# Performance work log

Measured on AMD Instinct MI355X. Metric: run time of the kernel, lower is better.

## Reference

```python
import jax, jax.numpy as jnp
import numpy as np
import math

N_HEAD = 16
V_HEAD = 32   # v_head_dim
NOPE = 32     # nope_head_dim
ROPE_D = 64   # rope_head_dim
KEEP = 256    # num_tokens_to_keep
EPS = 1e-6


def _freqs(T, dim=ROPE_D, theta=10000.0):
    f = 1.0 / (theta ** (jnp.arange(0, dim, 2, dtype=jnp.float32) / dim))
    t = jnp.arange(T, dtype=jnp.float32)
    a = jnp.outer(t, f)  # [T, dim//2]
    return jnp.cos(a), jnp.sin(a)


def _rope(x, cos, sin):
    # x: [B,H,S,D]; half-split rotation as in apply_rope
    S = x.shape[-2]
    c = cos[:S][None, None]
    s = sin[:S][None, None]
    x1, x2 = jnp.split(x, 2, axis=-1)
    return jnp.concatenate([x1 * c - x2 * s, x1 * s + x2 * c], axis=-1)


def _rms(x, g, eps=EPS):
    return x * jax.lax.rsqrt(jnp.mean(x * x, axis=-1, keepdims=True) + eps) * g


def _attn(q, k, v, causal):
    scale = 1.0 / math.sqrt(q.shape[-1])
    s = jnp.einsum('bhqd,bhkd->bhqk', q, k) * scale
    if causal:
        Tq, Tk = s.shape[-2], s.shape[-1]
        mask = jnp.tril(jnp.ones((Tq, Tk), dtype=bool))
        s = jnp.where(mask, s, jnp.finfo(s.dtype).min)
    return jnp.einsum('bhqk,bhkd->bhqd', jax.nn.softmax(s, axis=-1), v)


def _forward(x, w_cq, g_qnorm, w_dq_nope, w_dq_rope, w_ckv, g_kvnorm,
             w_dk_nope, w_dv, w_krope, w_imp, w_selk, w_selv,
             w_wink, w_winv, w_gate, w_proj):
    B, T, C = x.shape
    cos, sin = _freqs(T)

    # --- MLA query path ---
    nq = _rms(x @ w_cq, g_qnorm)                                  # [B,T,96]
    q_nope = (nq @ w_dq_nope).reshape(B, T, N_HEAD, NOPE).transpose(0, 2, 1, 3)
    q_rope = (nq @ w_dq_rope).reshape(B, T, N_HEAD, ROPE_D).transpose(0, 2, 1, 3)
    q_rope = _rope(q_rope, cos, sin)
    q = jnp.concatenate([q_nope, q_rope], axis=-1)                # [B,H,T,96]

    # --- branch gate ---
    gate = jax.nn.softmax((x @ w_gate).mean(axis=1), axis=-1)     # [B,3]

    # --- branch 1: MLA-compressed full KV ---
    ckv = _rms(x @ w_ckv, g_kvnorm)                               # [B,T,32]
    k_nope = (ckv @ w_dk_nope).reshape(B, T, N_HEAD, NOPE).transpose(0, 2, 1, 3)
    v1 = (ckv @ w_dv).reshape(B, T, N_HEAD, V_HEAD).transpose(0, 2, 1, 3)
    k_rope = (x @ w_krope).reshape(B, T, 1, ROPE_D).transpose(0, 2, 1, 3) / N_HEAD
    k_rope = _rope(k_rope, cos, sin)
    k1 = jnp.concatenate(
        [k_nope, jnp.broadcast_to(k_rope, (B, N_HEAD, T, ROPE_D))], axis=-1)

    # --- branch 2: top-k selected tokens ---
    scores = (x @ w_imp)[..., 0]                                  # [B,T]
    _, idx = jax.lax.top_k(scores, KEEP)
    idx = jnp.sort(idx, axis=1)
    sel = jnp.take_along_axis(x, idx[:, :, None], axis=1)         # [B,S,C]
    ks = (sel @ w_selk).reshape(B, KEEP, N_HEAD, NOPE + ROPE_D).transpose(0, 2, 1, 3)
    vs = (sel @ w_selv).reshape(B, KEEP, N_HEAD, V_HEAD).transpose(0, 2, 1, 3)
    ks = jnp.concatenate([ks[..., :NOPE], _rope(ks[..., NOPE:], cos, sin)], axis=-1)

    # --- branch 3: sliding window (training mode -> full x) ---
    kw = (x @ w_wink).reshape(B, T, N_HEAD, NOPE + ROPE_D).transpose(0, 2, 1, 3)
    vw = (x @ w_winv).reshape(B, T, N_HEAD, V_HEAD).transpose(0, 2, 1, 3)
    kw = jnp.concatenate([kw[..., :NOPE], _rope(kw[..., NOPE:], cos, sin)], axis=-1)

    a1 = _attn(q, k1, v1, causal=True)
    a2 = _attn(q, ks, vs, causal=False)
    a3 = _attn(q, kw, vw, causal=True)

    g = gate[:, :, None, None, None]
    out = g[:, 0] * a1 + g[:, 1] * a2 + g[:, 2] * a3              # [B,H,T,Vd]
    out = out.transpose(0, 2, 1, 3).reshape(B, T, N_HEAD * V_HEAD)
    return out @ w_proj                                           # [B,T,C]


def setup_inputs() -> dict:
    key = jax.random.key(0)
    ks = jax.random.split(key, 20)
    B, T, C = 2, 1024, 1024
    q_lora, kv_lora = 96, 32
    std = 0.02
    def w(k, shape):
        return jax.random.normal(k, shape, dtype=jnp.float32) * std
    return {
        'x': jax.random.normal(ks[0], (B, T, C), dtype=jnp.float32),
        'w_cq': w(ks[1], (C, q_lora)),
        'g_qnorm': jnp.ones((q_lora,), jnp.float32),
        'w_dq_nope': w(ks[2], (q_lora, N_HEAD * NOPE)),
        'w_dq_rope': w(ks[3], (q_lora, N_HEAD * ROPE_D)),
        'w_ckv': w(ks[4], (C, kv_lora)),
        'g_kvnorm': jnp.ones((kv_lora,), jnp.float32),
        'w_dk_nope': w(ks[5], (kv_lora, N_HEAD * NOPE)),
        'w_dv': w(ks[6], (kv_lora, N_HEAD * V_HEAD)),
        'w_krope': w(ks[7], (C, ROPE_D)),
        'w_imp': w(ks[8], (C, 1)),
        'w_selk': w(ks[9], (C, N_HEAD * (NOPE + ROPE_D))),
        'w_selv': w(ks[10], (C, N_HEAD * V_HEAD)),
        'w_wink': w(ks[11], (C, N_HEAD * (NOPE + ROPE_D))),
        'w_winv': w(ks[12], (C, N_HEAD * V_HEAD)),
        'w_gate': w(ks[13], (C, 3)),
        'w_proj': w(ks[14], (N_HEAD * V_HEAD, C)),
    }


def reference(x, w_cq, g_qnorm, w_dq_nope, w_dq_rope, w_ckv, g_kvnorm,
              w_dk_nope, w_dv, w_krope, w_imp, w_selk, w_selv,
              w_wink, w_winv, w_gate, w_proj):
    return _forward(x, w_cq, g_qnorm, w_dq_nope, w_dq_rope, w_ckv, g_kvnorm,
                    w_dk_nope, w_dv, w_krope, w_imp, w_selk, w_selv,
                    w_wink, w_winv, w_gate, w_proj)
```

## Files before the change

kernel.cpp:

```cpp
#include <hip/hip_runtime.h>
#include <math.h>

#define T_SEQ   1024
#define BATCH   2
#define CDIM    1024
#define NHEAD   16
#define VHEAD   32
#define KEEP    256
#define HEAD_D  96
#define SCALE_ATTN 0.1020620726159658f

#define BQ   64
#define BKT  64
#define SK   100
#define SPT  66
#define SPV  36

#define GBK 16
#define SA  132

#define XWW    2244
#define C_CQ   0
#define C_CKV  96
#define C_KRO  128
#define C_WINK 192
#define C_WINV 1728
#define C_IMP  2240
#define C_GATE 2241

#define QKVW   2560
#define C_QN   0
#define C_QR   512
#define C_KN   1536
#define C_V1   2048

#define SKW  2048

__global__ __launch_bounds__(256) void gemm128(const float* __restrict__ A,
                                               const float* __restrict__ B,
                                               float* __restrict__ C,
                                               int M, int N, int K,
                                               int lda, int ldb, int ldc,
                                               int kchunk) {
    __shared__ float As[GBK][SA];
    __shared__ float Bs[GBK][SA];
    int t = threadIdx.x;
    int tx = t & 15, ty = t >> 4;
    int row0 = blockIdx.y * 128, col0 = blockIdx.x * 128;
    int kb = blockIdx.z * kchunk;
    int ke = min(K, kb + kchunk);
    float acc[8][8] = {};

    for (int k0 = kb; k0 < ke; k0 += GBK) {
#pragma unroll
        for (int r = 0; r < 2; r++) {
            int idx = t + 256 * r;
            int row = idx >> 2, k4 = idx & 3;
            int gr = row0 + row;
            float4 v = make_float4(0.f, 0.f, 0.f, 0.f);
            if (gr < M) v = *(const float4*)&A[(size_t)gr * lda + k0 + k4 * 4];
            As[k4 * 4 + 0][row] = v.x;
            As[k4 * 4 + 1][row] = v.y;
            As[k4 * 4 + 2][row] = v.z;
            As[k4 * 4 + 3][row] = v.w;
        }
#pragma unroll
        for (int r = 0; r < 2; r++) {
            int idx = t + 256 * r;
            int kk = idx >> 5, n4 = idx & 31;
            int gc = col0 + n4 * 4;
            float4 v = make_float4(0.f, 0.f, 0.f, 0.f);
            if (gc + 3 < N) {
                v = *(const float4*)&B[(size_t)(k0 + kk) * ldb + gc];
            } else if (gc < N) {
                const float* bp = &B[(size_t)(k0 + kk) * ldb];
                float tmp[4] = {0.f, 0.f, 0.f, 0.f};
                for (int j = 0; j < 4 && gc + j < N; j++) tmp[j] = bp[gc + j];
                v = make_float4(tmp[0], tmp[1], tmp[2], tmp[3]);
            }
            *(float4*)&Bs[kk][n4 * 4] = v;
        }
        __syncthreads();
#pragma unroll
        for (int kk = 0; kk < GBK; kk++) {
            float4 a0 = *(float4*)&As[kk][ty * 4];
            float4 a1 = *(float4*)&As[kk][64 + ty * 4];
            float4 b0 = *(float4*)&Bs[kk][tx * 4];
            float4 b1 = *(float4*)&Bs[kk][64 + tx * 4];
            float av[8] = {a0.x, a0.y, a0.z, a0.w, a1.x, a1.y, a1.z, a1.w};
            float bv[8] = {b0.x, b0.y, b0.z, b0.w, b1.x, b1.y, b1.z, b1.w};
#pragma unroll
            for (int i = 0; i < 8; i++)
#pragma unroll
                for (int j = 0; j < 8; j++) acc[i][j] += av[i] * bv[j];
        }
        __syncthreads();
    }

    bool split = (gridDim.z > 1);
#pragma unroll
    for (int i = 0; i < 8; i++) {
        int gr = row0 + ((i < 4) ? (ty * 4 + i) : (64 + ty * 4 + (i - 4)));
        if (gr >= M) continue;
#pragma unroll
        for (int half = 0; half < 2; half++) {
            int gc = col0 + half * 64 + tx * 4;
            if (gc + 3 >= N) continue;
            float* cp = &C[(size_t)gr * ldc + gc];
            if (split) {
                atomicAdd(cp + 0, acc[i][half * 4 + 0]);
                atomicAdd(cp + 1, acc[i][half * 4 + 1]);
                atomicAdd(cp + 2, acc[i][half * 4 + 2]);
                atomicAdd(cp + 3, acc[i][half * 4 + 3]);
            } else {
                *(float4*)cp = make_float4(acc[i][half * 4 + 0], acc[i][half * 4 + 1],
                                           acc[i][half * 4 + 2], acc[i][half * 4 + 3]);
            }
        }
    }
}

__global__ void build_tab(float2* __restrict__ tab) {
    int idx = blockIdx.x * blockDim.x + threadIdx.x;
    if (idx >= T_SEQ * 32) return;
    int pos = idx >> 5, i = idx & 31;
    float expo = (float)i * (1.0f / 32.0f);
    float f = 1.0f / powf(10000.0f, expo);
    float a = (float)pos * f;
    float s, c;
    sincosf(a, &s, &c);
    tab[idx] = make_float2(c, s);
}

__global__ void pack_all(float* __restrict__ Bxw, float* __restrict__ Bqkv,
                         float* __restrict__ Bsel,
                         const float* __restrict__ cq, const float* __restrict__ ckv,
                         const float* __restrict__ kro, const float* __restrict__ wink,
                         const float* __restrict__ winv, const float* __restrict__ imp,
                         const float* __restrict__ gate,
                         const float* __restrict__ dqn, const float* __restrict__ dqr,
                         const float* __restrict__ dkn, const float* __restrict__ dv,
                         const float* __restrict__ selk, const float* __restrict__ selv) {
    int blk = blockIdx.x;
    if (blk < 1024) {
        int r = blk;
        for (int c = threadIdx.x; c < XWW; c += blockDim.x) {
            float v;
            if      (c < C_CKV)  v = cq  [(size_t)r * 96   + c];
            else if (c < C_KRO)  v = ckv [(size_t)r * 32   + (c - C_CKV)];
            else if (c < C_WINK) v = kro [(size_t)r * 64   + (c - C_KRO)];
            else if (c < C_WINV) v = wink[(size_t)r * 1536 + (c - C_WINK)];
            else if (c < C_IMP)  v = winv[(size_t)r * 512  + (c - C_WINV)];
            else if (c < C_GATE) v = imp [(size_t)r * 1    + (c - C_IMP)];
            else                 v = gate[(size_t)r * 3    + (c - C_GATE)];
            Bxw[(size_t)r * XWW + c] = v;
        }
    } else if (blk < 1152) {
        int r = blk - 1024;
        for (int c = threadIdx.x; c < QKVW; c += blockDim.x) {
            float v = 0.f;
            if (r < 96) {
                if (c < C_QR)      v = dqn[(size_t)r * 512 + c];
                else if (c < C_KN) v = dqr[(size_t)r * 1024 + (c - C_QR)];
            } else {
                if (c >= C_KN && c < C_V1) v = dkn[(size_t)(r - 96) * 512 + (c - C_KN)];
                else if (c >= C_V1)        v = dv [(size_t)(r - 96) * 512 + (c - C_V1)];
            }
            Bqkv[(size_t)r * QKVW + c] = v;
        }
    } else {
        int r = blk - 1152;
        for (int c = threadIdx.x; c < SKW; c += blockDim.x) {
            float v = (c < 1536) ? selk[(size_t)r * 1536 + c]
                                 : selv[(size_t)r * 512 + (c - 1536)];
            Bsel[(size_t)r * SKW + c] = v;
        }
    }
}

__global__ void xw_post(float* __restrict__ XW, const float* __restrict__ gq,
                        const float* __restrict__ gkv,
                        const float2* __restrict__ tab) {
    int row = blockIdx.x;
    int t = threadIdx.x;
    int w = t >> 6, lane = t & 63;
    float* rp = XW + (size_t)row * XWW;
    int pos = row & (T_SEQ - 1);
    const float2* tp = tab + pos * 32;

    if (w == 0) {
        float ss = 0.f;
        for (int d = lane; d < 96; d += 64) { float v = rp[d]; ss += v * v; }
        for (int off = 32; off; off >>= 1) ss += __shfl_xor(ss, off, 64);
        float r = rsqrtf(ss / 96.0f + 1e-6f);
        for (int d = lane; d < 96; d += 64) rp[d] *= r * gq[d];
    } else if (w == 1) {
        float ss = 0.f;
        for (int d = lane; d < 32; d += 64) { float v = rp[C_CKV + d]; ss += v * v; }
        for (int off = 32; off; off >>= 1) ss += __shfl_xor(ss, off, 64);
        float r = rsqrtf(ss / 32.0f + 1e-6f);
        for (int d = lane; d < 32; d += 64) rp[C_CKV + d] *= r * gkv[d];
    } else if (w == 2) {
        if (lane < 32) {
            float2 cs = tp[lane];
            float v1 = rp[C_KRO + lane], v2 = rp[C_KRO + 32 + lane];
            rp[C_KRO + lane]      = (v1 * cs.x - v2 * cs.y) * (1.0f / NHEAD);
            rp[C_KRO + 32 + lane] = (v1 * cs.y + v2 * cs.x) * (1.0f / NHEAD);
        }
    }
#pragma unroll
    for (int j = 0; j < 2; j++) {
        int item = t + j * 256;
        int h = item >> 5, i = item & 31;
        float2 cs = tp[i];
        size_t base = (size_t)(C_WINK + 32) + h * 96;
        float v1 = rp[base + i], v2 = rp[base + 32 + i];
        rp[base + i]      = v1 * cs.x - v2 * cs.y;
        rp[base + 32 + i] = v1 * cs.y + v2 * cs.x;
    }
}

__global__ void rope_tab(float* __restrict__ buf, int nrows, int rstride,
                         int nheads, int hstride, int roff, int posmod,
                         const float2* __restrict__ tab) {
    int total = nrows * nheads * 32;
    for (int it = blockIdx.x * blockDim.x + threadIdx.x; it < total;
         it += gridDim.x * blockDim.x) {
        int i = it & 31;
        int hr = it >> 5;
        int h = hr % nheads;
        int row = hr / nheads;
        int pos = row % posmod;
        float2 cs = tab[pos * 32 + i];
        size_t base = (size_t)row * rstride + (size_t)h * hstride + roff;
        float v1 = buf[base + i], v2 = buf[base + 32 + i];
        buf[base + i]      = v1 * cs.x - v2 * cs.y;
        buf[base + 32 + i] = v1 * cs.y + v2 * cs.x;
    }
}

__global__ void topk_gate(const float* __restrict__ xw, int* __restrict__ idx,
                          float* __restrict__ gate) {
    int b = blockIdx.x;
    __shared__ float s[1024];
    __shared__ int ps[1024];
    __shared__ float gred[3][16];
    int t = threadIdx.x;
    const float* rowp = &xw[((size_t)b * T_SEQ + t) * XWW];
    s[t] = rowp[C_IMP];
    float g0 = rowp[C_GATE + 0], g1 = rowp[C_GATE + 1], g2 = rowp[C_GATE + 2];
    for (int off = 32; off; off >>= 1) {
        g0 += __shfl_xor(g0, off, 64);
        g1 += __shfl_xor(g1, off, 64);
        g2 += __shfl_xor(g2, off, 64);
    }
    if ((t & 63) == 0) { int w = t >> 6; gred[0][w] = g0; gred[1][w] = g1; gred[2][w] = g2; }
    __syncthreads();
    if (t == 0) {
        float v0 = 0.f, v1 = 0.f, v2 = 0.f;
        for (int w = 0; w < 16; w++) { v0 += gred[0][w]; v1 += gred[1][w]; v2 += gred[2][w]; }
        v0 /= (float)T_SEQ; v1 /= (float)T_SEQ; v2 /= (float)T_SEQ;
        float m = fmaxf(v0, fmaxf(v1, v2));
        float e0 = expf(v0 - m), e1 = expf(v1 - m), e2 = expf(v2 - m);
        float ssum = e0 + e1 + e2;
        gate[b * 3 + 0] = e0 / ssum;
        gate[b * 3 + 1] = e1 / ssum;
        gate[b * 3 + 2] = e2 / ssum;
    }
    __syncthreads();
    float mine = s[t];
    int rank = 0;
    for (int j = 0; j < 1024; j++) {
        float v = s[j];
        rank += (v > mine) || (v == mine && j < t);
    }
    int selv = (rank < KEEP) ? 1 : 0;
    ps[t] = selv;
    __syncthreads();
    for (int off = 1; off < 1024; off <<= 1) {
        int add = (t >= off) ? ps[t - off] : 0;
        __syncthreads();
        ps[t] += add;
        __syncthreads();
    }
    if (selv) idx[b * KEEP + ps[t] - 1] = t;
}

__global__ void gather_sel(const float* __restrict__ x, const int* __restrict__ idx,
                           float* __restrict__ sel) {
    for (size_t i = (size_t)blockIdx.x * blockDim.x + threadIdx.x;
         i < (size_t)BATCH * KEEP * CDIM; i += (size_t)gridDim.x * blockDim.x) {
        int c = (int)(i & (CDIM - 1));
        int r = (int)((i >> 10) & (KEEP - 1));
        int b = (int)(i >> 18);
        sel[i] = x[((size_t)b * T_SEQ + idx[b * KEEP + r]) * CDIM + c];
    }
}

__global__ __launch_bounds__(512, 4) void flash_fused(
    const float* __restrict__ qkv, const float* __restrict__ xw,
    const float* __restrict__ skv, const float* __restrict__ gate,
    float* __restrict__ out) {
    __shared__ float Qs[BQ * SK];
    __shared__ float Ks[BKT * SK];
    __shared__ float Vs[BKT * SPV];
    __shared__ float Pt[BKT * SPT];

    int b = blockIdx.z, h = blockIdx.y;
    int qt = blockIdx.x;
    if (b == 1) qt = (gridDim.x - 1) - qt;
    int q0 = qt * BQ;
    int t = threadIdx.x;
    int tq = t >> 4, tk = t & 15;

    for (int i = t; i < BQ * 24; i += 512) {
        int row = i / 24, d4 = i % 24;
        size_t rq = (size_t)b * T_SEQ + q0 + row;
        float4 v;
        if (d4 < 8) v = *(const float4*)&qkv[rq * QKVW + C_QN + h * 32 + d4 * 4];
        else        v = *(const float4*)&qkv[rq * QKVW + C_QR + h * 64 + (d4 - 8) * 4];
        *(float4*)&Qs[row * SK + d4 * 4] = v;
    }

    int qq0 = q0 + 2 * tq, qq1 = qq0 + 1;
    float comb[2][2] = {};
    for (int phase = 0; phase < 3; phase++) {
        bool causal = (phase != 1);
        int ntiles = causal ? (qt + 1) : (KEEP / BKT);
        float m0 = -1e30f, m1 = -1e30f, l0 = 0.f, l1 = 0.f;
        float o00 = 0.f, o01 = 0.f, o10 = 0.f, o11 = 0.f;

        for (int kt = 0; kt < ntiles; kt++) {
            int j0 = kt * BKT;
            __syncthreads();

            for (int i = t; i < BKT * 24; i += 512) {
                int row = i / 24, d4 = i % 24;
                int j = j0 + row;
                float4 v;
                if (phase == 0) {
                    size_t rk = (size_t)b * T_SEQ + j;
                    if (d4 < 8) v = *(const float4*)&qkv[rk * QKVW + C_KN + h * 32 + d4 * 4];
                    else        v = *(const float4*)&xw[rk * XWW + C_KRO + (d4 - 8) * 4];
                } else if (phase == 1) {
                    v = *(const float4*)&skv[((size_t)b * KEEP + j) * SKW + h * 96 + d4 * 4];
                } else {
                    v = *(const float4*)&xw[((size_t)b * T_SEQ + j) * XWW + C_WINK + h * 96 + d4 * 4];
                }
                *(float4*)&Ks[row * SK + d4 * 4] = v;
            }
            for (int i = t; i < BKT * 8; i += 512) {
                int row = i >> 3, d4 = i & 7;
                int j = j0 + row;
                float4 v;
                if (phase == 0)      v = *(const float4*)&qkv[((size_t)b * T_SEQ + j) * QKVW + C_V1 + h * 32 + d4 * 4];
                else if (phase == 1) v = *(const float4*)&skv[((size_t)b * KEEP  + j) * SKW + 1536 + h * 32 + d4 * 4];
                else                 v = *(const float4*)&xw[((size_t)b * T_SEQ + j) * XWW + C_WINV + h * 32 + d4 * 4];
                *(float4*)&Vs[row * SPV + d4 * 4] = v;
            }
            __syncthreads();

            float s0[4] = {}, s1[4] = {};
#pragma unroll 6
            for (int d = 0; d < HEAD_D; d += 4) {
                float4 qa = *(float4*)&Qs[(2 * tq)     * SK + d];
                float4 qb = *(float4*)&Qs[(2 * tq + 1) * SK + d];
#pragma unroll
                for (int j = 0; j < 4; j++) {
                    float4 kv = *(float4*)&Ks[(16 * j + tk) * SK + d];
                    s0[j] += qa.x * kv.x + qa.y * kv.y + qa.z * kv.z + qa.w * kv.w;
                    s1[j] += qb.x * kv.x + qb.y * kv.y + qb.z * kv.z + qb.w * kv.w;
                }
            }
            float mt0 = -1e30f, mt1 = -1e30f;
#pragma unroll
            for (int j = 0; j < 4; j++) {
                int kk = j0 + 16 * j + tk;
                s0[j] *= SCALE_ATTN;
                s1[j] *= SCALE_ATTN;
                if (causal && kk > qq0) s0[j] = -1e30f;
                if (causal && kk > qq1) s1[j] = -1e30f;
                mt0 = fmaxf(mt0, s0[j]);
                mt1 = fmaxf(mt1, s1[j]);
            }
#pragma unroll
            for (int off = 1; off <= 8; off <<= 1) {
                mt0 = fmaxf(mt0, __shfl_xor(mt0, off, 64));
                mt1 = fmaxf(mt1, __shfl_xor(mt1, off, 64));
            }
            float mn0 = fmaxf(m0, mt0), mn1 = fmaxf(m1, mt1);
            float a0 = __expf(m0 - mn0), a1 = __expf(m1 - mn1);
            m0 = mn0; m1 = mn1;

            float rs0 = 0.f, rs1 = 0.f;
#pragma unroll
            for (int j = 0; j < 4; j++) {
                float p0 = __expf(s0[j] - mn0);
                float p1 = __expf(s1[j] - mn1);
                rs0 += p0; rs1 += p1;
                *(float2*)&Pt[(16 * j + tk) * SPT + 2 * tq] = make_float2(p0, p1);
            }
#pragma unroll
            for (int off = 1; off <= 8; off <<= 1) {
                rs0 += __shfl_xor(rs0, off, 64);
                rs1 += __shfl_xor(rs1, off, 64);
            }
            l0 = l0 * a0 + rs0;
            l1 = l1 * a1 + rs1;

            o00 *= a0; o01 *= a0; o10 *= a1; o11 *= a1;
#pragma unroll 8
            for (int kk = 0; kk < BKT; kk++) {
                float2 pv = *(float2*)&Pt[kk * SPT + 2 * tq];
                float2 vv = *(float2*)&Vs[kk * SPV + 2 * tk];
                o00 += pv.x * vv.x; o01 += pv.x * vv.y;
                o10 += pv.y * vv.x; o11 += pv.y * vv.y;
            }
        }

        float g = gate[b * 3 + phase];
        float i0 = g / l0, i1 = g / l1;
        comb[0][0] += o00 * i0; comb[0][1] += o01 * i0;
        comb[1][0] += o10 * i1; comb[1][1] += o11 * i1;
    }

    size_t r0 = ((size_t)b * T_SEQ + q0 + 2 * tq) * 512 + h * 32 + 2 * tk;
    out[r0]           = comb[0][0];
    out[r0 + 1]       = comb[0][1];
    out[r0 + 512]     = comb[1][0];
    out[r0 + 512 + 1] = comb[1][1];
}

extern "C" void kernel_launch(void* const* d_in, const int* in_sizes, int n_in,
                              void* d_out, int out_size, void* d_ws, size_t ws_size,
                              hipStream_t stream) {
    const float* x        = (const float*)d_in[0];
    const float* w_cq     = (const float*)d_in[1];
    const float* g_qnorm  = (const float*)d_in[2];
    const float* w_dqn    = (const float*)d_in[3];
    const float* w_dqr    = (const float*)d_in[4];
    const float* w_ckv    = (const float*)d_in[5];
    const float* g_kvnorm = (const float*)d_in[6];
    const float* w_dkn    = (const float*)d_in[7];
    const float* w_dv     = (const float*)d_in[8];
    const float* w_krope  = (const float*)d_in[9];
    const float* w_imp    = (const float*)d_in[10];
    const float* w_selk   = (const float*)d_in[11];
    const float* w_selv   = (const float*)d_in[12];
    const float* w_wink   = (const float*)d_in[13];
    const float* w_winv   = (const float*)d_in[14];
    const float* w_gate   = (const float*)d_in[15];
    const float* w_proj   = (const float*)d_in[16];
    float* out = (float*)d_out;

    const int BT = BATCH * T_SEQ;
    const int BS = BATCH * KEEP;

    float* ws = (float*)d_ws;
    size_t o = 0;
    float* XW     = ws + o; o += (size_t)BT * XWW;
    float* QKV    = ws + o; o += (size_t)BT * QKVW;
    float* skv    = ws + o; o += (size_t)BS * SKW;
    float* selb   = ws + o; o += (size_t)BS * CDIM;
    float* attn   = ws + o; o += (size_t)BT * 512;
    float* Bxw    = ws + o; o += (size_t)CDIM * XWW;
    float* Bqkv   = ws + o; o += (size_t)128 * QKVW;
    float* Bsel   = ws + o; o += (size_t)CDIM * SKW;
    float2* tab   = (float2*)(ws + o); o += (size_t)T_SEQ * 32 * 2;
    float* gatef  = ws + o; o += 8;
    int*   idx    = (int*)(ws + o); o += 512;

    auto gemm = [&](const float* A, const float* Bm, float* C, int M, int N, int K,
                    int lda, int ldb, int ldc, int ksplit = 1) {
        int kchunk = (K / ksplit + GBK - 1) / GBK * GBK;
        dim3 grid((N + 127) / 128, (M + 127) / 128, ksplit);
        gemm128<<<grid, 256, 0, stream>>>(A, Bm, C, M, N, K, lda, ldb, ldc, kchunk);
    };

    hipMemsetAsync(skv, 0, (size_t)BS * SKW * sizeof(float), stream);
    hipMemsetAsync(out, 0, (size_t)BT * CDIM * sizeof(float), stream);

    pack_all<<<2176, 256, 0, stream>>>(Bxw, Bqkv, Bsel,
                                       w_cq, w_ckv, w_krope, w_wink, w_winv,
                                       w_imp, w_gate,
                                       w_dqn, w_dqr, w_dkn, w_dv, w_selk, w_selv);
    build_tab<<<64, 512, 0, stream>>>(tab);

    gemm(x, Bxw, XW, BT, XWW, CDIM, CDIM, XWW, XWW);

    xw_post<<<BT, 256, 0, stream>>>(XW, g_qnorm, g_kvnorm, tab);

    topk_gate<<<BATCH, 1024, 0, stream>>>(XW, idx, gatef);
    gather_sel<<<2048, 256, 0, stream>>>(x, idx, selb);

    gemm(XW, Bqkv, QKV, BT, QKVW, 128, XWW, QKVW, QKVW);
    rope_tab<<<2048, 256, 0, stream>>>(QKV, BT, QKVW, 16, 64, C_QR, T_SEQ, tab);

    gemm(selb, Bsel, skv, BS, SKW, CDIM, CDIM, SKW, SKW, 4);
    rope_tab<<<512, 256, 0, stream>>>(skv, BS, SKW, 16, 96, 32, KEEP, tab);

    dim3 fgrid(T_SEQ / BQ, NHEAD, BATCH);
    flash_fused<<<fgrid, 512, 0, stream>>>(QKV, XW, skv, gatef, attn);

    gemm(attn, w_proj, out, BT, CDIM, 512, 512, CDIM, CDIM, 2);
}
```

Baseline: 955.5 us.

## Fuse gather, rope and table build into GEMM, flash and pack kernels

The selected-token gather is folded into the GEMM's A-row loads through an index array, so the separate gather kernel and its buffer go away. The two rope passes over QKV and the selected K are dropped, and the rotation is applied on the fly while Q and the selected-K tiles are loaded in the flash kernel. The sincos table build moves into extra blocks of pack_all. This cuts kernel launches and global round trips, at the cost of extra loads and arithmetic inside the flash kernel's load loops.

```diff
diff --git a/kernel.cpp b/kernel.cpp
--- a/kernel.cpp
+++ b/kernel.cpp
@@ -41,7 +41,9 @@
                                                float* __restrict__ C,
                                                int M, int N, int K,
                                                int lda, int ldb, int ldc,
-                                               int kchunk) {
+                                               int kchunk,
+                                               const int* __restrict__ Arowidx,
+                                               int rowdiv, int rowmul) {
     __shared__ float As[GBK][SA];
     __shared__ float Bs[GBK][SA];
     int t = threadIdx.x;
@@ -51,14 +53,25 @@
     int ke = min(K, kb + kchunk);
     float acc[8][8] = {};
 
+    int asrc[2]; bool aok[2];
+#pragma unroll
+    for (int r = 0; r < 2; r++) {
+        int idx = t + 256 * r;
+        int row = idx >> 2;
+        int gr = row0 + row;
+        aok[r] = (gr < M);
+        int ar = gr;
+        if (Arowidx != nullptr && aok[r]) ar = (gr / rowdiv) * rowmul + Arowidx[gr];
+        asrc[r] = ar;
+    }
+
     for (int k0 = kb; k0 < ke; k0 += GBK) {
 #pragma unroll
         for (int r = 0; r < 2; r++) {
             int idx = t + 256 * r;
             int row = idx >> 2, k4 = idx & 3;
-            int gr = row0 + row;
             float4 v = make_float4(0.f, 0.f, 0.f, 0.f);
-            if (gr < M) v = *(const float4*)&A[(size_t)gr * lda + k0 + k4 * 4];
+            if (aok[r]) v = *(const float4*)&A[(size_t)asrc[r] * lda + k0 + k4 * 4];
             As[k4 * 4 + 0][row] = v.x;
             As[k4 * 4 + 1][row] = v.y;
             As[k4 * 4 + 2][row] = v.z;
@@ -120,20 +133,8 @@
     }
 }
 
-__global__ void build_tab(float2* __restrict__ tab) {
-    int idx = blockIdx.x * blockDim.x + threadIdx.x;
-    if (idx >= T_SEQ * 32) return;
-    int pos = idx >> 5, i = idx & 31;
-    float expo = (float)i * (1.0f / 32.0f);
-    float f = 1.0f / powf(10000.0f, expo);
-    float a = (float)pos * f;
-    float s, c;
-    sincosf(a, &s, &c);
-    tab[idx] = make_float2(c, s);
-}
-
 __global__ void pack_all(float* __restrict__ Bxw, float* __restrict__ Bqkv,
-                         float* __restrict__ Bsel,
+                         float* __restrict__ Bsel, float2* __restrict__ tab,
                          const float* __restrict__ cq, const float* __restrict__ ckv,
                          const float* __restrict__ kro, const float* __restrict__ wink,
                          const float* __restrict__ winv, const float* __restrict__ imp,
@@ -168,12 +169,23 @@
             }
             Bqkv[(size_t)r * QKVW + c] = v;
         }
-    } else {
+    } else if (blk < 2176) {
         int r = blk - 1152;
         for (int c = threadIdx.x; c < SKW; c += blockDim.x) {
             float v = (c < 1536) ? selk[(size_t)r * 1536 + c]
                                  : selv[(size_t)r * 512 + (c - 1536)];
             Bsel[(size_t)r * SKW + c] = v;
+        }
+    } else {
+        int idx = (blk - 2176) * 256 + threadIdx.x;
+        if (idx < T_SEQ * 32) {
+            int pos = idx >> 5, i = idx & 31;
+            float expo = (float)i * (1.0f / 32.0f);
+            float f = 1.0f / powf(10000.0f, expo);
+            float a = (float)pos * f;
+            float s, c;
+            sincosf(a, &s, &c);
+            tab[idx] = make_float2(c, s);
         }
     }
 }
@@ -220,25 +232,6 @@
     }
 }
 
-__global__ void rope_tab(float* __restrict__ buf, int nrows, int rstride,
-                         int nheads, int hstride, int roff, int posmod,
-                         const float2* __restrict__ tab) {
-    int total = nrows * nheads * 32;
-    for (int it = blockIdx.x * blockDim.x + threadIdx.x; it < total;
-         it += gridDim.x * blockDim.x) {
-        int i = it & 31;
-        int hr = it >> 5;
-        int h = hr % nheads;
-        int row = hr / nheads;
-        int pos = row % posmod;
-        float2 cs = tab[pos * 32 + i];
-        size_t base = (size_t)row * rstride + (size_t)h * hstride + roff;
-        float v1 = buf[base + i], v2 = buf[base + 32 + i];
-        buf[base + i]      = v1 * cs.x - v2 * cs.y;
-        buf[base + 32 + i] = v1 * cs.y + v2 * cs.x;
-    }
-}
-
 __global__ void topk_gate(const float* __restrict__ xw, int* __restrict__ idx,
                           float* __restrict__ gate) {
     int b = blockIdx.x;
@@ -286,21 +279,10 @@
     if (selv) idx[b * KEEP + ps[t] - 1] = t;
 }
 
-__global__ void gather_sel(const float* __restrict__ x, const int* __restrict__ idx,
-                           float* __restrict__ sel) {
-    for (size_t i = (size_t)blockIdx.x * blockDim.x + threadIdx.x;
-         i < (size_t)BATCH * KEEP * CDIM; i += (size_t)gridDim.x * blockDim.x) {
-        int c = (int)(i & (CDIM - 1));
-        int r = (int)((i >> 10) & (KEEP - 1));
-        int b = (int)(i >> 18);
-        sel[i] = x[((size_t)b * T_SEQ + idx[b * KEEP + r]) * CDIM + c];
-    }
-}
-
 __global__ __launch_bounds__(512, 4) void flash_fused(
     const float* __restrict__ qkv, const float* __restrict__ xw,
     const float* __restrict__ skv, const float* __restrict__ gate,
-    float* __restrict__ out) {
+    const float2* __restrict__ tab, float* __restrict__ out) {
     __shared__ float Qs[BQ * SK];
     __shared__ float Ks[BKT * SK];
     __shared__ float Vs[BKT * SPV];
@@ -317,8 +299,27 @@
         int row = i / 24, d4 = i % 24;
         size_t rq = (size_t)b * T_SEQ + q0 + row;
         float4 v;
-        if (d4 < 8) v = *(const float4*)&qkv[rq * QKVW + C_QN + h * 32 + d4 * 4];
-        else        v = *(const float4*)&qkv[rq * QKVW + C_QR + h * 64 + (d4 - 8) * 4];
+        if (d4 < 8) {
+            v = *(const float4*)&qkv[rq * QKVW + C_QN + h * 32 + d4 * 4];
+        } else {
+            const float* qb = &qkv[rq * QKVW + C_QR + h * 64];
+            int dd = d4 - 8;
+            float4 a = *(const float4*)&qb[dd * 4];
+            const float2* tp = tab + (size_t)(q0 + row) * 32;
+            if (dd < 8) {
+                float4 p = *(const float4*)&qb[(dd + 8) * 4];
+                int i0 = dd * 4;
+                float2 c0 = tp[i0], c1 = tp[i0 + 1], c2 = tp[i0 + 2], c3 = tp[i0 + 3];
+                v = make_float4(a.x * c0.x - p.x * c0.y, a.y * c1.x - p.y * c1.y,
+                                a.z * c2.x - p.z * c2.y, a.w * c3.x - p.w * c3.y);
+            } else {
+                float4 p = *(const float4*)&qb[(dd - 8) * 4];
+                int i0 = (dd - 8) * 4;
+                float2 c0 = tp[i0], c1 = tp[i0 + 1], c2 = tp[i0 + 2], c3 = tp[i0 + 3];
+                v = make_float4(p.x * c0.y + a.x * c0.x, p.y * c1.y + a.y * c1.x,
+                                p.z * c2.y + a.z * c2.x, p.w * c3.y + a.w * c3.x);
+            }
+        }
         *(float4*)&Qs[row * SK + d4 * 4] = v;
     }
 
@@ -343,7 +344,27 @@
                     if (d4 < 8) v = *(const float4*)&qkv[rk * QKVW + C_KN + h * 32 + d4 * 4];
                     else        v = *(const float4*)&xw[rk * XWW + C_KRO + (d4 - 8) * 4];
                 } else if (phase == 1) {
-                    v = *(const float4*)&skv[((size_t)b * KEEP + j) * SKW + h * 96 + d4 * 4];
+                    const float* kb2 = &skv[((size_t)b * KEEP + j) * SKW + h * 96];
+                    if (d4 < 8) {
+                        v = *(const float4*)&kb2[d4 * 4];
+                    } else {
+                        int dd = d4 - 8;
+                        float4 a = *(const float4*)&kb2[d4 * 4];
+                        const float2* tp = tab + (size_t)j * 32;
+                        if (dd < 8) {
+                            float4 p = *(const float4*)&kb2[(d4 + 8) * 4];
+                            int i0 = dd * 4;
+                            float2 c0 = tp[i0], c1 = tp[i0 + 1], c2 = tp[i0 + 2], c3 = tp[i0 + 3];
+                            v = make_float4(a.x * c0.x - p.x * c0.y, a.y * c1.x - p.y * c1.y,
+                                            a.z * c2.x - p.z * c2.y, a.w * c3.x - p.w * c3.y);
+                        } else {
+                            float4 p = *(const float4*)&kb2[(d4 - 8) * 4];
+                            int i0 = (dd - 8) * 4;
+                            float2 c0 = tp[i0], c1 = tp[i0 + 1], c2 = tp[i0 + 2], c3 = tp[i0 + 3];
+                            v = make_float4(p.x * c0.y + a.x * c0.x, p.y * c1.y + a.y * c1.x,
+                                            p.z * c2.y + a.z * c2.x, p.w * c3.y + a.w * c3.x);
+                        }
+                    }
                 } else {
                     v = *(const float4*)&xw[((size_t)b * T_SEQ + j) * XWW + C_WINK + h * 96 + d4 * 4];
                 }
@@ -461,7 +482,6 @@
     float* XW     = ws + o; o += (size_t)BT * XWW;
     float* QKV    = ws + o; o += (size_t)BT * QKVW;
     float* skv    = ws + o; o += (size_t)BS * SKW;
-    float* selb   = ws + o; o += (size_t)BS * CDIM;
     float* attn   = ws + o; o += (size_t)BT * 512;
     float* Bxw    = ws + o; o += (size_t)CDIM * XWW;
     float* Bqkv   = ws + o; o += (size_t)128 * QKVW;
@@ -471,36 +491,34 @@
     int*   idx    = (int*)(ws + o); o += 512;
 
     auto gemm = [&](const float* A, const float* Bm, float* C, int M, int N, int K,
-                    int lda, int ldb, int ldc, int ksplit = 1) {
+                    int lda, int ldb, int ldc, int ksplit = 1,
+                    const int* Arowidx = nullptr, int rowdiv = 1, int rowmul = 1) {
         int kchunk = (K / ksplit + GBK - 1) / GBK * GBK;
         dim3 grid((N + 127) / 128, (M + 127) / 128, ksplit);
-        gemm128<<<grid, 256, 0, stream>>>(A, Bm, C, M, N, K, lda, ldb, ldc, kchunk);
+        gemm128<<<grid, 256, 0, stream>>>(A, Bm, C, M, N, K, lda, ldb, ldc, kchunk,
+                                          Arowidx, rowdiv, rowmul);
     };
 
     hipMemsetAsync(skv, 0, (size_t)BS * SKW * sizeof(float), stream);
     hipMemsetAsync(out, 0, (size_t)BT * CDIM * sizeof(float), stream);
 
-    pack_all<<<2176, 256, 0, stream>>>(Bxw, Bqkv, Bsel,
+    pack_all<<<2304, 256, 0, stream>>>(Bxw, Bqkv, Bsel, tab,
                                        w_cq, w_ckv, w_krope, w_wink, w_winv,
                                        w_imp, w_gate,
                                        w_dqn, w_dqr, w_dkn, w_dv, w_selk, w_selv);
-    build_tab<<<64, 512, 0, stream>>>(tab);
 
     gemm(x, Bxw, XW, BT, XWW, CDIM, CDIM, XWW, XWW);
 
     xw_post<<<BT, 256, 0, stream>>>(XW, g_qnorm, g_kvnorm, tab);
 
     topk_gate<<<BATCH, 1024, 0, stream>>>(XW, idx, gatef);
-    gather_sel<<<2048, 256, 0, stream>>>(x, idx, selb);
 
     gemm(XW, Bqkv, QKV, BT, QKVW, 128, XWW, QKVW, QKVW);
-    rope_tab<<<2048, 256, 0, stream>>>(QKV, BT, QKVW, 16, 64, C_QR, T_SEQ, tab);
-
-    gemm(selb, Bsel, skv, BS, SKW, CDIM, CDIM, SKW, SKW, 4);
-    rope_tab<<<512, 256, 0, stream>>>(skv, BS, SKW, 16, 96, 32, KEEP, tab);
+
+    gemm(x, Bsel, skv, BS, SKW, CDIM, CDIM, SKW, SKW, 4, idx, KEEP, T_SEQ);
 
     dim3 fgrid(T_SEQ / BQ, NHEAD, BATCH);
-    flash_fused<<<fgrid, 512, 0, stream>>>(QKV, XW, skv, gatef, attn);
+    flash_fused<<<fgrid, 512, 0, stream>>>(QKV, XW, skv, gatef, tab, attn);
 
     gemm(attn, w_proj, out, BT, CDIM, 512, 512, CDIM, CDIM, 2);
 }
```

After: 953.7 us. No clear change (-0.2%).
